# Performance work log

Measured on AMD Instinct MI355X. Metric: run time of the kernel, lower is better.

Reference implementation:

```python
import jax, jax.numpy as jnp
import numpy as np

E, K, D_IN, D_OUT, D_HID = 16, 2, 1024, 1024, 2048

def setup_inputs() -> dict:
    key = jax.random.key(0)
    ks = jax.random.split(key, 6)
    s_in = 1.0 / np.sqrt(D_IN)
    s_hid = 1.0 / np.sqrt(D_HID)
    return {
        "x": jax.random.normal(ks[0], (4096, D_IN), dtype=jnp.float32),
        "gate_w": jax.random.uniform(ks[1], (E, D_IN), jnp.float32, -s_in, s_in),
        "w1": jax.random.uniform(ks[2], (E, D_HID, D_IN), jnp.float32, -s_in, s_in),
        "b1": jax.random.uniform(ks[3], (E, D_HID), jnp.float32, -s_in, s_in),
        "w2": jax.random.uniform(ks[4], (E, D_OUT, D_HID), jnp.float32, -s_hid, s_hid),
        "b2": jax.random.uniform(ks[5], (E, D_OUT), jnp.float32, -s_hid, s_hid),
    }

def reference(x, gate_w, w1, b1, w2, b2):
    # gate: [B, E]
    gate_scores = jnp.einsum('bi,ei->be', x, gate_w)
    topk_vals, topk_idxs = jax.lax.top_k(gate_scores, K)  # [B, K]
    topk_weights = jax.nn.softmax(topk_vals, axis=-1)     # [B, K]
    # dense all-expert MLP (faithful to reference): [B, E, D_OUT]
    h = jax.nn.relu(jnp.einsum('bi,ehi->beh', x, w1) + b1[None])
    expert_outputs = jnp.einsum('beh,eoh->beo', h, w2) + b2[None]
    # gather selected experts: [B, K, D_OUT]
    sel = jnp.take_along_axis(expert_outputs, topk_idxs[:, :, None], axis=1)
    return jnp.sum(sel * topk_weights[:, :, None], axis=1)
```

## Files before the change

### kernel.cpp

```cpp
#include <hip/hip_runtime.h>
#include <hip/hip_bf16.h>
#include <math.h>

#define B_TOK 4096
#define NE 16
#define DI 1024
#define DH 2048
#define DOUT 1024
#define NSLOT (B_TOK * 2)

typedef unsigned short u16;
typedef short bfrag __attribute__((ext_vector_type(8)));
typedef float f32x4 __attribute__((ext_vector_type(4)));
typedef u16 u16x8 __attribute__((ext_vector_type(8)));

__device__ __forceinline__ u16 f2bf(float f) {
    union { float f; unsigned u; } v; v.f = f;
    return (u16)((v.u + 0x7fffu + ((v.u >> 16) & 1u)) >> 16);
}

__device__ __forceinline__ void async16(const void* g, void* lds) {
    __builtin_amdgcn_global_load_lds(
        (const __attribute__((address_space(1))) void*)g,
        (__attribute__((address_space(3))) void*)lds,
        16, 0, 0);
}

__global__ void zero_init(float* __restrict__ out, int n4) {
    int i = blockIdx.x * blockDim.x + threadIdx.x;
    if (i < n4) ((float4*)out)[i] = make_float4(0.f, 0.f, 0.f, 0.f);
}

__global__ void convert_bf16(const float* __restrict__ src, u16* __restrict__ dst, int n8) {
    int i = blockIdx.x * blockDim.x + threadIdx.x;
    if (i >= n8) return;
    const float4* s4 = (const float4*)src;
    float4 a = s4[2 * i], b = s4[2 * i + 1];
    u16x8 r;
    r[0] = f2bf(a.x); r[1] = f2bf(a.y); r[2] = f2bf(a.z); r[3] = f2bf(a.w);
    r[4] = f2bf(b.x); r[5] = f2bf(b.y); r[6] = f2bf(b.z); r[7] = f2bf(b.w);
    ((u16x8*)dst)[i] = r;
}

__global__ __launch_bounds__(256) void gate_topk(
    const float* __restrict__ x, const float* __restrict__ gw,
    int* __restrict__ token_e, float* __restrict__ token_w)
{
    int wave = threadIdx.x >> 6, lane = threadIdx.x & 63;
    int t = blockIdx.x * 4 + wave;
    const float4* x4 = (const float4*)(x + (size_t)t * DI);
    const float4* g4 = (const float4*)gw;
    double acc[NE];
#pragma unroll
    for (int e = 0; e < NE; ++e) acc[e] = 0.0;
#pragma unroll
    for (int i = 0; i < 4; ++i) {
        float4 xv = x4[lane + i * 64];
#pragma unroll
        for (int e = 0; e < NE; ++e) {
            float4 gv = g4[e * 256 + lane + i * 64];
            acc[e] += (double)xv.x * gv.x + (double)xv.y * gv.y
                    + (double)xv.z * gv.z + (double)xv.w * gv.w;
        }
    }
#pragma unroll
    for (int e = 0; e < NE; ++e) {
        double v = acc[e];
        for (int off = 32; off; off >>= 1) v += __shfl_xor(v, off, 64);
        acc[e] = v;
    }
    if (lane == 0) {
        int e0 = 0; double v0 = acc[0];
#pragma unroll
        for (int e = 1; e < NE; ++e) if (acc[e] > v0) { v0 = acc[e]; e0 = e; }
        int e1 = -1; double v1 = -1e300;
#pragma unroll
        for (int e = 0; e < NE; ++e) if (e != e0 && acc[e] > v1) { v1 = acc[e]; e1 = e; }
        float d = expf((float)(v1 - v0));
        float w0 = 1.f / (1.f + d);
        float w1 = d * w0;
        token_e[2 * t] = e0; token_e[2 * t + 1] = e1;
        token_w[2 * t] = w0; token_w[2 * t + 1] = w1;
    }
}

__global__ __launch_bounds__(1024) void route(
    const int* __restrict__ token_e, const float* __restrict__ token_w,
    int* __restrict__ counts, int* __restrict__ offsets,
    int* __restrict__ slot_token, float* __restrict__ slot_wgt)
{
    __shared__ int lcnt[NE];
    __shared__ int lcur[NE];
    int tid = threadIdx.x;
    if (tid < NE) lcnt[tid] = 0;
    __syncthreads();
    for (int i = tid; i < NSLOT; i += 1024) atomicAdd(&lcnt[token_e[i]], 1);
    __syncthreads();
    if (tid == 0) {
        int s = 0;
        for (int e = 0; e < NE; ++e) {
            int c = lcnt[e];
            counts[e] = c; offsets[e] = s; lcur[e] = s; s += c;
        }
    }
    __syncthreads();
    for (int i = tid; i < NSLOT; i += 1024) {
        int e = token_e[i];
        int pos = atomicAdd(&lcur[e], 1);
        slot_token[pos] = i >> 1;
        slot_wgt[pos] = token_w[i];
    }
}

template <int PHASE>
__global__ __launch_bounds__(256) void moe_gemm(
    const u16* __restrict__ Abuf,
    const u16* __restrict__ Bbuf,
    const float* __restrict__ bias,
    const int* __restrict__ counts, const int* __restrict__ offsets,
    const int* __restrict__ slot_token, const float* __restrict__ slot_wgt,
    u16* __restrict__ hb, float* __restrict__ out)
{
    constexpr int KDIM = (PHASE == 1) ? DI : DH;
    constexpr int NDIM = (PHASE == 1) ? DH : DOUT;

    const int e = blockIdx.z;
    const int cnt = counts[e];
    const int m0 = blockIdx.y * 128;
    if (m0 >= cnt) return;
    const int n0 = blockIdx.x * 128;
    const int sbase = offsets[e];

    __shared__ u16 ldsbuf[16384];
    u16* alds = ldsbuf;
    u16* blds = ldsbuf + 8192;

    const int tid = threadIdx.x;
    const int wv = tid >> 6, lane = tid & 63;
    const int lrow = lane >> 3;
    const int lkc = lane & 7;
    const int skc = lkc ^ lrow;

    const u16* aptr[4]; const u16* bptr[4];
    const u16* bbase = Bbuf + (size_t)e * NDIM * KDIM;
#pragma unroll
    for (int r = 0; r < 4; ++r) {
        int arow = m0 + r * 32 + wv * 8 + lrow;
        if (PHASE == 1) {
            int c = cnt - 1; if (arow > c) arow = c;
            aptr[r] = Abuf + (size_t)slot_token[sbase + arow] * KDIM + skc * 8;
        } else {
            int s = sbase + arow; if (s > NSLOT - 1) s = NSLOT - 1;
            aptr[r] = Abuf + (size_t)s * KDIM + skc * 8;
        }
        int brow = n0 + r * 32 + wv * 8 + lrow;
        bptr[r] = bbase + (size_t)brow * KDIM + skc * 8;
    }

    f32x4 acc[4][4];
#pragma unroll
    for (int i = 0; i < 4; ++i)
#pragma unroll
        for (int j = 0; j < 4; ++j) acc[i][j] = (f32x4){0.f, 0.f, 0.f, 0.f};

    const int wm = (wv & 1) * 64, wn = (wv >> 1) * 64;
    const int quad = lane >> 4, mr = lane & 15;
    const int msw = mr & 7;

    const int nk = KDIM / 64;
    for (int kt = 0; kt < nk; ++kt) {
        __syncthreads();
#pragma unroll
        for (int r = 0; r < 4; ++r) {
            async16(aptr[r] + kt * 64, alds + (r * 32 + wv * 8) * 64);
            async16(bptr[r] + kt * 64, blds + (r * 32 + wv * 8) * 64);
        }
        __syncthreads();
#pragma unroll
        for (int kk = 0; kk < 2; ++kk) {
            bfrag af[4], bf[4];
            const int ch = ((kk * 4 + quad) ^ msw) * 8;
#pragma unroll
            for (int i = 0; i < 4; ++i) af[i] = *(const bfrag*)(alds + (wm + i * 16 + mr) * 64 + ch);
#pragma unroll
            for (int j = 0; j < 4; ++j) bf[j] = *(const bfrag*)(blds + (wn + j * 16 + mr) * 64 + ch);
#pragma unroll
            for (int i = 0; i < 4; ++i)
#pragma unroll
                for (int j = 0; j < 4; ++j)
                    acc[i][j] = __builtin_amdgcn_mfma_f32_16x16x32_bf16(af[i], bf[j], acc[i][j], 0, 0, 0);
        }
    }

    const float* bias_e = bias + e * NDIM;
    if constexpr (PHASE == 1) {
#pragma unroll
        for (int i = 0; i < 4; ++i) {
            int mbase = wm + i * 16 + quad * 4;
#pragma unroll
            for (int j = 0; j < 4; ++j) {
                int n = n0 + wn + j * 16 + mr;
                float bv = bias_e[n];
#pragma unroll
                for (int r = 0; r < 4; ++r) {
                    int m = m0 + mbase + r;
                    if (m < cnt) {
                        float v = acc[i][j][r] + bv;
                        v = v > 0.f ? v : 0.f;
                        hb[(size_t)(sbase + m) * DH + n] = f2bf(v);
                    }
                }
            }
        }
    } else {
#pragma unroll
        for (int i = 0; i < 4; ++i) {
            int mbase = wm + i * 16 + quad * 4;
#pragma unroll
            for (int r = 0; r < 4; ++r) {
                int m = m0 + mbase + r;
                if (m < cnt) {
                    int slot = sbase + m;
                    int tok = slot_token[slot];
                    float wgt = slot_wgt[slot];
                    float* orow = out + (size_t)tok * DOUT + n0 + wn;
#pragma unroll
                    for (int j = 0; j < 4; ++j) {
                        int nl = j * 16 + mr;
                        float v = wgt * (acc[i][j][r] + bias_e[n0 + wn + nl]);
                        atomicAdd(orow + nl, v);
                    }
                }
            }
        }
    }
}

extern "C" void kernel_launch(void* const* d_in, const int* in_sizes, int n_in,
                              void* d_out, int out_size, void* d_ws, size_t ws_size,
                              hipStream_t stream) {
    const float* x  = (const float*)d_in[0];
    const float* gw = (const float*)d_in[1];
    const float* w1 = (const float*)d_in[2];
    const float* b1 = (const float*)d_in[3];
    const float* w2 = (const float*)d_in[4];
    const float* b2 = (const float*)d_in[5];
    float* out = (float*)d_out;

    char* ws = (char*)d_ws;
    u16* xb = (u16*)ws;
    u16* wb = (u16*)(ws + 8388608);
    u16* hb = (u16*)(ws + 8388608 + 67108864);
    char* rb = ws + 109051904;
    int*   counts     = (int*)(rb);
    int*   offsets    = (int*)(rb + 64);
    int*   token_e    = (int*)(rb + 192);
    float* token_w    = (float*)(rb + 192 + 32768);
    int*   slot_token = (int*)(rb + 192 + 65536);
    float* slot_wgt   = (float*)(rb + 192 + 98304);

    zero_init<<<4096, 256, 0, stream>>>(out, (B_TOK * DOUT) / 4);
    convert_bf16<<<2048, 256, 0, stream>>>(x, xb, (B_TOK * DI) / 8);
    convert_bf16<<<16384, 256, 0, stream>>>(w1, wb, (NE * DH * DI) / 8);
    gate_topk<<<1024, 256, 0, stream>>>(x, gw, token_e, token_w);
    route<<<1, 1024, 0, stream>>>(token_e, token_w, counts, offsets, slot_token, slot_wgt);
    moe_gemm<1><<<dim3(DH / 128, B_TOK / 128, NE), 256, 0, stream>>>(
        xb, wb, b1, counts, offsets, slot_token, slot_wgt, hb, out);
    convert_bf16<<<16384, 256, 0, stream>>>(w2, wb, (NE * DOUT * DH) / 8);
    moe_gemm<2><<<dim3(DOUT / 128, B_TOK / 128, NE), 256, 0, stream>>>(
        hb, wb, b2, counts, offsets, slot_token, slot_wgt, hb, out);
}
```

Before: 567.4 us.

## Triple-buffer MoE GEMM K-loop with async prefetch and fuse x conversion into gating

Result: faster. 515.6 us (-9.1%).

```diff
diff --git a/kernel.cpp b/kernel.cpp
--- a/kernel.cpp
+++ b/kernel.cpp
@@ -44,18 +44,21 @@
 
 __global__ __launch_bounds__(256) void gate_topk(
     const float* __restrict__ x, const float* __restrict__ gw,
-    int* __restrict__ token_e, float* __restrict__ token_w)
+    int* __restrict__ token_e, float* __restrict__ token_w, u16* __restrict__ xb)
 {
     int wave = threadIdx.x >> 6, lane = threadIdx.x & 63;
     int t = blockIdx.x * 4 + wave;
     const float4* x4 = (const float4*)(x + (size_t)t * DI);
     const float4* g4 = (const float4*)gw;
+    ushort4* xb4 = (ushort4*)(xb + (size_t)t * DI);
     double acc[NE];
 #pragma unroll
     for (int e = 0; e < NE; ++e) acc[e] = 0.0;
 #pragma unroll
     for (int i = 0; i < 4; ++i) {
         float4 xv = x4[lane + i * 64];
+        ushort4 c; c.x = f2bf(xv.x); c.y = f2bf(xv.y); c.z = f2bf(xv.z); c.w = f2bf(xv.w);
+        xb4[lane + i * 64] = c;
 #pragma unroll
         for (int e = 0; e < NE; ++e) {
             float4 gv = g4[e * 256 + lane + i * 64];
@@ -123,6 +126,7 @@
 {
     constexpr int KDIM = (PHASE == 1) ? DI : DH;
     constexpr int NDIM = (PHASE == 1) ? DH : DOUT;
+    constexpr int nk = KDIM / 32;
 
     const int e = blockIdx.z;
     const int cnt = counts[e];
@@ -131,31 +135,31 @@
     const int n0 = blockIdx.x * 128;
     const int sbase = offsets[e];
 
-    __shared__ u16 ldsbuf[16384];
-    u16* alds = ldsbuf;
-    u16* blds = ldsbuf + 8192;
+    __shared__ u16 ldsbuf[3 * 8192];
 
     const int tid = threadIdx.x;
     const int wv = tid >> 6, lane = tid & 63;
-    const int lrow = lane >> 3;
-    const int lkc = lane & 7;
-    const int skc = lkc ^ lrow;
-
-    const u16* aptr[4]; const u16* bptr[4];
+    const int lrow = lane >> 2;
+    const int lkc = lane & 3;
+    const int skc = lkc ^ ((lrow >> 1) & 3);
+
+    const u16* aptr[2]; const u16* bptr[2];
     const u16* bbase = Bbuf + (size_t)e * NDIM * KDIM;
 #pragma unroll
-    for (int r = 0; r < 4; ++r) {
-        int arow = m0 + r * 32 + wv * 8 + lrow;
+    for (int rd = 0; rd < 2; ++rd) {
+        int arow = m0 + rd * 64 + wv * 16 + lrow;
         if (PHASE == 1) {
             int c = cnt - 1; if (arow > c) arow = c;
-            aptr[r] = Abuf + (size_t)slot_token[sbase + arow] * KDIM + skc * 8;
+            aptr[rd] = Abuf + (size_t)slot_token[sbase + arow] * KDIM + skc * 8;
         } else {
             int s = sbase + arow; if (s > NSLOT - 1) s = NSLOT - 1;
-            aptr[r] = Abuf + (size_t)s * KDIM + skc * 8;
-        }
-        int brow = n0 + r * 32 + wv * 8 + lrow;
-        bptr[r] = bbase + (size_t)brow * KDIM + skc * 8;
-    }
+            aptr[rd] = Abuf + (size_t)s * KDIM + skc * 8;
+        }
+        int brow = n0 + rd * 64 + wv * 16 + lrow;
+        bptr[rd] = bbase + (size_t)brow * KDIM + skc * 8;
+    }
+    const int slab0 = wv * 512;
+    const int slab1 = 2048 + wv * 512;
 
     f32x4 acc[4][4];
 #pragma unroll
@@ -165,31 +169,44 @@
 
     const int wm = (wv & 1) * 64, wn = (wv >> 1) * 64;
     const int quad = lane >> 4, mr = lane & 15;
-    const int msw = mr & 7;
-
-    const int nk = KDIM / 64;
-    for (int kt = 0; kt < nk; ++kt) {
-        __syncthreads();
-#pragma unroll
-        for (int r = 0; r < 4; ++r) {
-            async16(aptr[r] + kt * 64, alds + (r * 32 + wv * 8) * 64);
-            async16(bptr[r] + kt * 64, blds + (r * 32 + wv * 8) * 64);
-        }
-        __syncthreads();
-#pragma unroll
-        for (int kk = 0; kk < 2; ++kk) {
-            bfrag af[4], bf[4];
-            const int ch = ((kk * 4 + quad) ^ msw) * 8;
-#pragma unroll
-            for (int i = 0; i < 4; ++i) af[i] = *(const bfrag*)(alds + (wm + i * 16 + mr) * 64 + ch);
-#pragma unroll
-            for (int j = 0; j < 4; ++j) bf[j] = *(const bfrag*)(blds + (wn + j * 16 + mr) * 64 + ch);
-#pragma unroll
-            for (int i = 0; i < 4; ++i)
-#pragma unroll
-                for (int j = 0; j < 4; ++j)
-                    acc[i][j] = __builtin_amdgcn_mfma_f32_16x16x32_bf16(af[i], bf[j], acc[i][j], 0, 0, 0);
-        }
+    const int ach = (quad ^ ((mr >> 1) & 3)) * 8;
+    const int aro = (wm + mr) * 32 + ach;
+    const int bro = 4096 + (wn + mr) * 32 + ach;
+
+#pragma unroll
+    for (int p = 0; p < 2; ++p) {
+        u16* base = ldsbuf + p * 8192;
+        async16(aptr[0] + p * 32, base + slab0);
+        async16(aptr[1] + p * 32, base + slab1);
+        async16(bptr[0] + p * 32, base + 4096 + slab0);
+        async16(bptr[1] + p * 32, base + 4096 + slab1);
+    }
+
+    int cb = 0;
+    for (int k = 0; k < nk; ++k) {
+        if (k + 1 < nk) __builtin_amdgcn_s_waitcnt(0x0F74);
+        else            __builtin_amdgcn_s_waitcnt(0x0F70);
+        __builtin_amdgcn_s_barrier();
+        if (k + 2 < nk) {
+            int nb = cb + 2; if (nb >= 3) nb -= 3;
+            u16* base = ldsbuf + nb * 8192;
+            async16(aptr[0] + (k + 2) * 32, base + slab0);
+            async16(aptr[1] + (k + 2) * 32, base + slab1);
+            async16(bptr[0] + (k + 2) * 32, base + 4096 + slab0);
+            async16(bptr[1] + (k + 2) * 32, base + 4096 + slab1);
+        }
+        const u16* sb = ldsbuf + cb * 8192;
+        bfrag af[4], bf[4];
+#pragma unroll
+        for (int i = 0; i < 4; ++i) af[i] = *(const bfrag*)(sb + aro + i * 512);
+#pragma unroll
+        for (int j = 0; j < 4; ++j) bf[j] = *(const bfrag*)(sb + bro + j * 512);
+#pragma unroll
+        for (int i = 0; i < 4; ++i)
+#pragma unroll
+            for (int j = 0; j < 4; ++j)
+                acc[i][j] = __builtin_amdgcn_mfma_f32_16x16x32_bf16(af[i], bf[j], acc[i][j], 0, 0, 0);
+        if (++cb == 3) cb = 0;
     }
 
     const float* bias_e = bias + e * NDIM;
@@ -260,9 +277,8 @@
     float* slot_wgt   = (float*)(rb + 192 + 98304);
 
     zero_init<<<4096, 256, 0, stream>>>(out, (B_TOK * DOUT) / 4);
-    convert_bf16<<<2048, 256, 0, stream>>>(x, xb, (B_TOK * DI) / 8);
+    gate_topk<<<1024, 256, 0, stream>>>(x, gw, token_e, token_w, xb);
     convert_bf16<<<16384, 256, 0, stream>>>(w1, wb, (NE * DH * DI) / 8);
-    gate_topk<<<1024, 256, 0, stream>>>(x, gw, token_e, token_w);
     route<<<1, 1024, 0, stream>>>(token_e, token_w, counts, offsets, slot_token, slot_wgt);
     moe_gemm<1><<<dim3(DH / 128, B_TOK / 128, NE), 256, 0, stream>>>(
         xb, wb, b1, counts, offsets, slot_token, slot_wgt, hb, out);
```
